# Kernel tuning notes

Measured on AMD Instinct MI355X. Metric: run time of the kernel, lower is better.

## Reference

```python
import jax, jax.numpy as jnp
import numpy as np
from jax import lax

DIM = 128; HEADS = 8; SPLIT = 4; MLP = 4
B = 8; H = 64; W = 64
EPS = 1e-5

def conv1x1(x, w, b):
    # x: (b,c,h,w), w: (o,c), b: (o,)
    return jnp.einsum('oc,bchw->bohw', w, x) + b[None, :, None, None]

def dwconv3(x, w, b):
    # depthwise 3x3, w: (C,1,3,3)
    c = x.shape[1]
    y = lax.conv_general_dilated(x, w, window_strides=(1, 1), padding=((1, 1), (1, 1)),
                                 feature_group_count=c,
                                 dimension_numbers=('NCHW', 'OIHW', 'NCHW'))
    return y + b[None, :, None, None]

def groupnorm1(x, g, bta):
    # GroupNorm with 1 group: normalize over (C,H,W) per sample
    mu = x.mean(axis=(1, 2, 3), keepdims=True)
    var = ((x - mu) ** 2).mean(axis=(1, 2, 3), keepdims=True)
    xn = (x - mu) * lax.rsqrt(var + EPS)
    return xn * g[None, :, None, None] + bta[None, :, None, None]

def eca(x, w):
    b, c, h, w_ = x.shape
    y = x.mean(axis=(2, 3))                         # (b,c)
    y = lax.conv_general_dilated(y[:, None, :], w, window_strides=(1,), padding=((2, 2),),
                                 dimension_numbers=('NCH', 'OIH', 'NCH'))  # (b,1,c)
    gate = jax.nn.sigmoid(y[:, 0])[:, :, None, None]
    return x * gate

def esa(x, alpha):
    x_se = x - x.mean(axis=(2, 3), keepdims=True)   # subtract per-channel GAP
    x_max = x_se.max(axis=1, keepdims=True)
    x_min = x_se.min(axis=1, keepdims=True)
    a = alpha[0]
    return x * jax.nn.sigmoid(x_max) * a + x * jax.nn.sigmoid(x_min) * (1.0 - a)

def eaa(q, k, v, h_sp, w_sp, cpe_w, cpe_b):
    b, c, h, w = q.shape
    hd = c // HEADS
    nh, nw = h // h_sp, w // w_sp
    L = h_sp * w_sp
    cpe = dwconv3(v, cpe_w, cpe_b)
    def win(t):
        t = t.reshape(b, c, nh, h_sp, nw, w_sp)
        t = t.transpose(0, 2, 4, 3, 5, 1).reshape(-1, L, HEADS, hd)
        return t.transpose(0, 2, 1, 3)  # (b*nh*nw, heads, L, hd)
    qw, kw, vw = win(q), win(k), win(v)
    attn = jax.nn.softmax(qw @ kw.transpose(0, 1, 3, 2), axis=-1)  # no scale, as in source
    o = attn @ vw                                    # (b*nh*nw, heads, L, hd)
    o = o.transpose(0, 2, 1, 3).reshape(b, nh, nw, h_sp, w_sp, c)
    o = o.transpose(0, 5, 1, 3, 2, 4).reshape(b, c, h, w)
    return o + cpe

def setup_inputs() -> dict:
    key = jax.random.key(0)
    ks = jax.random.split(key, 16)
    d = DIM
    z = lambda *s: jnp.zeros(s, jnp.float32)
    def n(i, shape, s=0.02):
        return jax.random.normal(ks[i], shape, dtype=jnp.float32) * s
    return dict(
        x=jax.random.normal(ks[0], (B, d, H, W), dtype=jnp.float32),
        eca_w=n(1, (1, 1, 5), 0.2),
        esa_alpha=jnp.ones((1,), jnp.float32),
        cpe1_w=n(2, (d, 1, 3, 3), 0.1), cpe1_b=z(d),
        g1=jnp.ones((d,), jnp.float32), b1=z(d),
        actp_w=n(3, (d, d)), actp_b=z(d),
        inp_w=n(4, (d, d)), inp_b=z(d),
        dwc_w=n(5, (d, 1, 3, 3), 0.1), dwc_b=z(d),
        qkv_w=n(6, (5 * d, d)), qkv_b=z(5 * d),
        eaax_w=n(7, (d, 1, 3, 3), 0.1), eaax_b=z(d),
        eaay_w=n(8, (d, 1, 3, 3), 0.1), eaay_b=z(d),
        outp_w=n(9, (d, d)), outp_b=z(d),
        cpe2_w=n(10, (d, 1, 3, 3), 0.1), cpe2_b=z(d),
        g2=jnp.ones((d,), jnp.float32), b2=z(d),
        mlp1_w=n(11, (MLP * d, d)), mlp1_b=z(MLP * d),
        mlp2_w=n(12, (d, MLP * d)), mlp2_b=z(d),
    )

def reference(x, eca_w, esa_alpha, cpe1_w, cpe1_b, g1, b1, actp_w, actp_b, inp_w, inp_b,
              dwc_w, dwc_b, qkv_w, qkv_b, eaax_w, eaax_b, eaay_w, eaay_b, outp_w, outp_b,
              cpe2_w, cpe2_b, g2, b2, mlp1_w, mlp1_b, mlp2_w, mlp2_b):
    b, c, h, w = x.shape
    x = eca(x, eca_w) + esa(x, esa_alpha)
    x = x + dwconv3(x, cpe1_w, cpe1_b)
    shortcut = x
    xn = groupnorm1(x, g1, b1)
    act_res = jax.nn.relu(conv1x1(xn, actp_w, actp_b))
    t = jax.nn.relu(dwconv3(conv1x1(xn, inp_w, inp_b), dwc_w, dwc_b))
    t = conv1x1(t, qkv_w, qkv_b)                     # (b, 5c, h, w)
    t5 = t.reshape(b, c, 5, h, w)                    # channel i::5 == t5[:,:,i]
    q0, k0, v0, q1, k1 = (t5[:, :, i] for i in range(5))
    a = eaa(q0, k0, v0, h, SPLIT, eaax_w, eaax_b) + eaa(q1, k1, v0, SPLIT, w, eaay_w, eaay_b)
    out = conv1x1(a * act_res, outp_w, outp_b) + shortcut
    out = out + dwconv3(out, cpe2_w, cpe2_b)
    mlp = conv1x1(jax.nn.relu(conv1x1(groupnorm1(out, g2, b2), mlp1_w, mlp1_b)), mlp2_w, mlp2_b)
    return mlp + out
```

## Files before the change

kernel.cpp:

```cpp
#include <hip/hip_runtime.h>

#define NPIX 4096
#define CDIM 128
#define BATCH 8
#define EPSN 1e-5f
#define LOG2E 1.44269504088896340736f

typedef __attribute__((ext_vector_type(8))) short short8;
typedef __attribute__((ext_vector_type(4))) float f32x4;
typedef __attribute__((ext_vector_type(16))) float f32x16;

__device__ __forceinline__ float sigmoidf_(float x) { return 1.f / (1.f + __expf(-x)); }

__device__ __forceinline__ unsigned short f2b(float f) {
    unsigned int u = __float_as_uint(f);
    unsigned int r = (u + 0x7FFF + ((u >> 16) & 1)) >> 16;
    return (unsigned short)r;
}
__device__ __forceinline__ float b2f(unsigned short u) {
    return __uint_as_float((unsigned int)u << 16);
}

__device__ __forceinline__ void pl32swap(unsigned int& a, unsigned int& b) {
    asm("v_permlane32_swap_b32 %0, %1" : "+v"(a), "+v"(b));
}

__device__ __forceinline__ int tok2pix(int mode, int wi, int l) {
    return (mode == 0) ? ((l >> 2) * 64 + wi * 4 + (l & 3))
                       : ((wi * 4 + (l >> 6)) * 64 + (l & 63));
}

__global__ __launch_bounds__(256) void convert_w_kernel(const float* __restrict__ qkv_w,
                                                        const float* __restrict__ mlp1_w,
                                                        const float* __restrict__ mlp2_w,
                                                        const float* __restrict__ actp_w,
                                                        const float* __restrict__ inp_w,
                                                        const float* __restrict__ outp_w,
                                                        const float* __restrict__ qkv_b,
                                                        const float* __restrict__ eaax_w,
                                                        const float* __restrict__ eaax_b,
                                                        const float* __restrict__ eaay_w,
                                                        const float* __restrict__ eaay_b,
                                                        const float* __restrict__ cpe1_w,
                                                        const float* __restrict__ dwc_w,
                                                        const float* __restrict__ cpe2_w,
                                                        const float* __restrict__ actp_b,
                                                        const float* __restrict__ inp_b,
                                                        unsigned short* __restrict__ dst,
                                                        float* __restrict__ qb_r,
                                                        float* __restrict__ wsT,
                                                        float* __restrict__ bsum,
                                                        float* __restrict__ cpe1T,
                                                        float* __restrict__ dwcT,
                                                        float* __restrict__ cpe2T,
                                                        float* __restrict__ abi,
                                                        float* __restrict__ gstats) {
    int i = blockIdx.x * 256 + threadIdx.x;
    if (i >= 267776) {
        if (i < 269824) gstats[i - 267776] = 0.f;
        return;
    }
    if (i < 262144) {
        float v;
        if (i < 81920) {
            int o = i >> 7, c = i & 127;
            int g = o >> 7;
            v = qkv_w[(size_t)(5 * (o & 127) + g) * 128 + c];
            if (g == 0 || g == 3) v *= LOG2E;
        } else if (i < 147456) v = mlp1_w[i - 81920];
        else if (i < 212992)   v = mlp2_w[i - 147456];
        else if (i < 229376)   v = actp_w[i - 212992];
        else if (i < 245760)   v = inp_w[i - 229376];
        else                   v = outp_w[i - 245760];
        dst[i] = f2b(v);
    } else {
        int j = i - 262144;
        if (j < 640) {
            int g = j >> 7;
            float v = qkv_b[5 * (j & 127) + g];
            if (g == 0 || g == 3) v *= LOG2E;
            qb_r[j] = v;
        }
        else if (j < 1792) {
            int idx = j - 640; int k = idx >> 7, c = idx & 127;
            wsT[idx] = eaax_w[c * 9 + k] + eaay_w[c * 9 + k];
        } else if (j < 1920) bsum[j - 1792] = eaax_b[j - 1792] + eaay_b[j - 1792];
        else if (j < 3072) {
            int idx = j - 1920; int k = idx >> 7, c = idx & 127;
            cpe1T[idx] = cpe1_w[c * 9 + k];
        } else if (j < 4224) {
            int idx = j - 3072; int k = idx >> 7, c = idx & 127;
            dwcT[idx] = dwc_w[c * 9 + k];
        } else if (j < 5376) {
            int idx = j - 4224; int k = idx >> 7, c = idx & 127;
            cpe2T[idx] = cpe2_w[c * 9 + k];
        } else {
            int idx = j - 5376;
            abi[idx] = (idx < 128) ? actp_b[idx] : inp_b[idx - 128];
        }
    }
}

__global__ __launch_bounds__(256) void mean_bc_kernel(const float* __restrict__ x,
                                                      float* __restrict__ mean) {
    __shared__ float sb[4];
    int bc = blockIdx.x;
    const float* p = x + (size_t)bc * NPIX;
    float s = 0.f;
    for (int i = threadIdx.x; i < NPIX; i += 256) s += p[i];
#pragma unroll
    for (int off = 32; off > 0; off >>= 1) s += __shfl_down(s, off, 64);
    if ((threadIdx.x & 63) == 0) sb[threadIdx.x >> 6] = s;
    __syncthreads();
    if (threadIdx.x == 0) mean[bc] = (sb[0] + sb[1] + sb[2] + sb[3]) * (1.f / (float)NPIX);
}

__global__ __launch_bounds__(256) void esa_tr_kernel(const float* __restrict__ x,
                                                     const float* __restrict__ mean,
                                                     const float* __restrict__ w5,
                                                     const float* __restrict__ alpha_p,
                                                     float* __restrict__ y) {
    __shared__ float tile[128][65];
    __shared__ float smx[4][64], smn[4][64], ssc[64], gat[128];
    int b = blockIdx.y, p0 = blockIdx.x * 64;
    int tx = threadIdx.x, pl = tx & 63, part = tx >> 6;
    const float* xb = x + (size_t)b * CDIM * NPIX;
    const float* mb = mean + b * CDIM;
    for (int c = part; c < CDIM; c += 4)
        tile[c][pl] = xb[(size_t)c * NPIX + p0 + pl];
    __syncthreads();
    float mx = -1e30f, mn = 1e30f;
#pragma unroll
    for (int cc = 0; cc < 32; ++cc) {
        int c = part * 32 + cc;
        float v = tile[c][pl] - mb[c];
        mx = fmaxf(mx, v); mn = fminf(mn, v);
    }
    smx[part][pl] = mx; smn[part][pl] = mn;
    __syncthreads();
    if (tx < 128) {
        float s = 0.f;
#pragma unroll
        for (int k = 0; k < 5; ++k) {
            int cc = tx + k - 2;
            if (cc >= 0 && cc < CDIM) s += w5[k] * mb[cc];
        }
        gat[tx] = sigmoidf_(s);
    }
    if (part == 0) {
        float m1 = fmaxf(fmaxf(smx[0][pl], smx[1][pl]), fmaxf(smx[2][pl], smx[3][pl]));
        float m2 = fminf(fminf(smn[0][pl], smn[1][pl]), fminf(smn[2][pl], smn[3][pl]));
        float a = alpha_p[0];
        ssc[pl] = sigmoidf_(m1) * a + sigmoidf_(m2) * (1.f - a);
    }
    __syncthreads();
    int c2 = tx & 127, pr = tx >> 7;
    float* yb = y + ((size_t)b * NPIX + p0) * CDIM;
    float gv = gat[c2];
    for (int p = pr; p < 64; p += 2)
        yb[(size_t)p * CDIM + c2] = tile[c2][p] * (gv + ssc[p]);
}

__global__ __launch_bounds__(256) void cpe_f32_kernel(const float* __restrict__ in,
                                                      const float* __restrict__ wT,
                                                      const float* __restrict__ bias,
                                                      float* __restrict__ out,
                                                      float* __restrict__ stats) {
    __shared__ float sb[8];
    int b = blockIdx.y, tx = threadIdx.x;
    int cg = tx & 15, pp = tx >> 4;
    int p = blockIdx.x * 16 + pp;
    int xx = p & 63, yy = p >> 6;
    int c0 = cg * 8;
    float acc[8], ctr[8];
#pragma unroll
    for (int j = 0; j < 8; ++j) acc[j] = bias[c0 + j];
#pragma unroll
    for (int dy = -1; dy <= 1; ++dy) {
        int y2 = yy + dy;
        if (y2 < 0 || y2 >= 64) continue;
#pragma unroll
        for (int dx = -1; dx <= 1; ++dx) {
            int x2 = xx + dx;
            if (x2 < 0 || x2 >= 64) continue;
            const float* ip = &in[((size_t)b * NPIX + y2 * 64 + x2) * 128 + c0];
            float4 v0 = *(const float4*)ip;
            float4 v1 = *(const float4*)(ip + 4);
            const float* wr = wT + ((dy + 1) * 3 + dx + 1) * 128 + c0;
            acc[0] += v0.x * wr[0]; acc[1] += v0.y * wr[1];
            acc[2] += v0.z * wr[2]; acc[3] += v0.w * wr[3];
            acc[4] += v1.x * wr[4]; acc[5] += v1.y * wr[5];
            acc[6] += v1.z * wr[6]; acc[7] += v1.w * wr[7];
            if (dy == 0 && dx == 0) {
                ctr[0] = v0.x; ctr[1] = v0.y; ctr[2] = v0.z; ctr[3] = v0.w;
                ctr[4] = v1.x; ctr[5] = v1.y; ctr[6] = v1.z; ctr[7] = v1.w;
            }
        }
    }
    float s = 0.f, s2 = 0.f;
    float r[8];
#pragma unroll
    for (int j = 0; j < 8; ++j) {
        r[j] = ctr[j] + acc[j];
        s += r[j]; s2 += r[j] * r[j];
    }
    float* op = &out[((size_t)b * NPIX + p) * 128 + c0];
    *(float4*)op = make_float4(r[0], r[1], r[2], r[3]);
    *(float4*)(op + 4) = make_float4(r[4], r[5], r[6], r[7]);
#pragma unroll
    for (int off = 32; off > 0; off >>= 1) {
        s += __shfl_down(s, off, 64);
        s2 += __shfl_down(s2, off, 64);
    }
    int wv = tx >> 6;
    if ((tx & 63) == 0) { sb[wv] = s; sb[4 + wv] = s2; }
    __syncthreads();
    if (tx == 0) {
        int slot = (b * 8 + (blockIdx.x & 7)) * 16;
        atomicAdd(&stats[slot], sb[0] + sb[1] + sb[2] + sb[3]);
        atomicAdd(&stats[slot + 1], sb[4] + sb[5] + sb[6] + sb[7]);
    }
}

__global__ __launch_bounds__(256) void dwc_bf16_kernel(const unsigned short* __restrict__ in,
                                                       const float* __restrict__ wT,
                                                       const float* __restrict__ bias,
                                                       unsigned short* __restrict__ out) {
    int b = blockIdx.y, tx = threadIdx.x;
    int cg = tx & 15, pp = tx >> 4;
    int p = blockIdx.x * 16 + pp;
    int xx = p & 63, yy = p >> 6;
    int c0 = cg * 8;
    float acc[8];
#pragma unroll
    for (int j = 0; j < 8; ++j) acc[j] = bias[c0 + j];
#pragma unroll
    for (int dy = -1; dy <= 1; ++dy) {
        int y2 = yy + dy;
        if (y2 < 0 || y2 >= 64) continue;
#pragma unroll
        for (int dx = -1; dx <= 1; ++dx) {
            int x2 = xx + dx;
            if (x2 < 0 || x2 >= 64) continue;
            unsigned short v[8];
            *(uint4*)v = *(const uint4*)&in[((size_t)b * NPIX + y2 * 64 + x2) * 128 + c0];
            const float* wr = wT + ((dy + 1) * 3 + dx + 1) * 128 + c0;
#pragma unroll
            for (int j = 0; j < 8; ++j) acc[j] += b2f(v[j]) * wr[j];
        }
    }
    unsigned short o[8];
#pragma unroll
    for (int j = 0; j < 8; ++j) o[j] = f2b(fmaxf(acc[j], 0.f));
    *(uint4*)&out[((size_t)b * NPIX + p) * 128 + c0] = *(uint4*)o;
}

__global__ __launch_bounds__(256) void conv_mfma_kernel(const unsigned short* __restrict__ in_t,
                                                        const float* __restrict__ in_f32,
                                                        const float* __restrict__ gst,
                                                        const float* __restrict__ gg,
                                                        const float* __restrict__ gbta,
                                                        const unsigned short* __restrict__ w,
                                                        const float* __restrict__ bias,
                                                        const float* __restrict__ res,
                                                        float* __restrict__ out,
                                                        unsigned short* __restrict__ out_t,
                                                        unsigned short* __restrict__ out_t2,
                                                        int Cin, int Cout, int relu, int nchw) {
    __shared__ __align__(16) unsigned short A_s[128][136];
    __shared__ __align__(16) unsigned short B_s[64][136];
    int b = blockIdx.z, p0 = blockIdx.x * 64, o0 = blockIdx.y * 128;
    int tx = threadIdx.x;
    int wave = tx >> 6, lane = tx & 63;
    int wm = wave & 1, wn = wave >> 1;
    int quad = lane >> 4, l16 = lane & 15;

    float mu = 0.f, rr = 1.f;
    if (in_f32) {
        float su = 0.f, sq = 0.f;
#pragma unroll
        for (int sl = 0; sl < 8; ++sl) {
            su += gst[(b * 8 + sl) * 16];
            sq += gst[(b * 8 + sl) * 16 + 1];
        }
        const float n = 1.f / (float)(CDIM * NPIX);
        mu = su * n;
        float var = sq * n - mu * mu;
        rr = rsqrtf(var + EPSN);
    }

    f32x4 acc[4][2];
#pragma unroll
    for (int mt = 0; mt < 4; ++mt) {
#pragma unroll
        for (int r = 0; r < 4; ++r) {
            float bv = bias[o0 + wm * 64 + mt * 16 + quad * 4 + r];
#pragma unroll
            for (int nt = 0; nt < 2; ++nt) acc[mt][nt][r] = bv;
        }
    }

    for (int k0 = 0; k0 < Cin; k0 += 128) {
#pragma unroll
        for (int j = 0; j < 8; ++j) {
            int idx = tx + 256 * j;
            int row = idx >> 4, c16 = idx & 15;
            *(uint4*)&A_s[row][c16 * 8] =
                *(const uint4*)&w[(size_t)(o0 + row) * Cin + k0 + c16 * 8];
        }
        if (in_f32) {
#pragma unroll
            for (int j = 0; j < 4; ++j) {
                int idx = tx + 256 * j;
                int row = idx >> 4, c16 = idx & 15;
                int ch = c16 * 8;
                const float* ip = &in_f32[((size_t)b * NPIX + p0 + row) * 128 + ch];
                float4 v0 = *(const float4*)ip;
                float4 v1 = *(const float4*)(ip + 4);
                unsigned short o[8];
                o[0] = f2b((v0.x - mu) * rr * gg[ch + 0] + gbta[ch + 0]);
                o[1] = f2b((v0.y - mu) * rr * gg[ch + 1] + gbta[ch + 1]);
                o[2] = f2b((v0.z - mu) * rr * gg[ch + 2] + gbta[ch + 2]);
                o[3] = f2b((v0.w - mu) * rr * gg[ch + 3] + gbta[ch + 3]);
                o[4] = f2b((v1.x - mu) * rr * gg[ch + 4] + gbta[ch + 4]);
                o[5] = f2b((v1.y - mu) * rr * gg[ch + 5] + gbta[ch + 5]);
                o[6] = f2b((v1.z - mu) * rr * gg[ch + 6] + gbta[ch + 6]);
                o[7] = f2b((v1.w - mu) * rr * gg[ch + 7] + gbta[ch + 7]);
                *(uint4*)&B_s[row][c16 * 8] = *(uint4*)o;
            }
        } else {
#pragma unroll
            for (int j = 0; j < 4; ++j) {
                int idx = tx + 256 * j;
                int row = idx >> 4, c16 = idx & 15;
                *(uint4*)&B_s[row][c16 * 8] =
                    *(const uint4*)&in_t[((size_t)b * NPIX + p0 + row) * Cin + k0 + c16 * 8];
            }
        }
        __syncthreads();
#pragma unroll
        for (int ks = 0; ks < 128; ks += 32) {
            short8 af[4], bf[2];
#pragma unroll
            for (int mt = 0; mt < 4; ++mt)
                af[mt] = *(const short8*)&A_s[wm * 64 + mt * 16 + l16][ks + quad * 8];
#pragma unroll
            for (int nt = 0; nt < 2; ++nt)
                bf[nt] = *(const short8*)&B_s[wn * 32 + nt * 16 + l16][ks + quad * 8];
#pragma unroll
            for (int mt = 0; mt < 4; ++mt)
#pragma unroll
                for (int nt = 0; nt < 2; ++nt)
                    acc[mt][nt] = __builtin_amdgcn_mfma_f32_16x16x32_bf16(
                        af[mt], bf[nt], acc[mt][nt], 0, 0, 0);
        }
        __syncthreads();
    }

    int dorelu = (relu == 1) || (relu == 2 && blockIdx.y == 0);
    if (out_t) {
#pragma unroll
        for (int mt = 0; mt < 4; ++mt) {
#pragma unroll
            for (int nt = 0; nt < 2; ++nt) {
                int p = p0 + wn * 32 + nt * 16 + l16;
                int ob = o0 + wm * 64 + mt * 16 + quad * 4;
                unsigned short* dbuf = out_t;
                int oc = ob;
                if (out_t2 && o0 >= 128) { dbuf = out_t2; oc = ob - 128; }
                ushort4 u;
                float v0 = acc[mt][nt][0], v1 = acc[mt][nt][1];
                float v2 = acc[mt][nt][2], v3 = acc[mt][nt][3];
                if (dorelu) { v0 = fmaxf(v0, 0.f); v1 = fmaxf(v1, 0.f);
                              v2 = fmaxf(v2, 0.f); v3 = fmaxf(v3, 0.f); }
                u.x = f2b(v0); u.y = f2b(v1); u.z = f2b(v2); u.w = f2b(v3);
                *(ushort4*)&dbuf[((size_t)b * NPIX + p) * Cout + oc] = u;
            }
        }
    } else if (!nchw) {
#pragma unroll
        for (int mt = 0; mt < 4; ++mt) {
#pragma unroll
            for (int nt = 0; nt < 2; ++nt) {
                int p = p0 + wn * 32 + nt * 16 + l16;
                int ob = o0 + wm * 64 + mt * 16 + quad * 4;
                size_t ix = ((size_t)b * NPIX + p) * Cout + ob;
                float4 v = make_float4(acc[mt][nt][0], acc[mt][nt][1],
                                       acc[mt][nt][2], acc[mt][nt][3]);
                if (dorelu) { v.x = fmaxf(v.x, 0.f); v.y = fmaxf(v.y, 0.f);
                              v.z = fmaxf(v.z, 0.f); v.w = fmaxf(v.w, 0.f); }
                if (res) {
                    float4 rv = *(const float4*)&res[ix];
                    v.x += rv.x; v.y += rv.y; v.z += rv.z; v.w += rv.w;
                }
                *(float4*)&out[ix] = v;
            }
        }
    } else {
        float* outb = out + (size_t)b * Cout * NPIX;
#pragma unroll
        for (int mt = 0; mt < 4; ++mt) {
#pragma unroll
            for (int nt = 0; nt < 2; ++nt) {
                int p = p0 + wn * 32 + nt * 16 + l16;
                int ob = o0 + wm * 64 + mt * 16 + quad * 4;
                float4 rv = make_float4(0.f, 0.f, 0.f, 0.f);
                if (res) rv = *(const float4*)&res[((size_t)b * NPIX + p) * 128 + ob];
#pragma unroll
                for (int r = 0; r < 4; ++r) {
                    float v = acc[mt][nt][r];
                    if (dorelu) v = fmaxf(v, 0.f);
                    v += (r == 0 ? rv.x : r == 1 ? rv.y : r == 2 ? rv.z : rv.w);
                    outb[(size_t)(ob + r) * NPIX + p] = v;
                }
            }
        }
    }
}

__global__ __launch_bounds__(256) void attn_dual_kernel(const unsigned short* __restrict__ t_t,
                                                        float* __restrict__ a0,
                                                        float* __restrict__ a1) {
    __shared__ __align__(16) unsigned short Vt[32][264];
    int wi = blockIdx.x, head = blockIdx.y;
    int z = blockIdx.z;
    int b = z >> 1, which = z & 1;
    int qoff = which ? 384 : 0;
    int koff = which ? 512 : 128;
    int mode = which;
    float* a_out = which ? a1 : a0;
    int tx = threadIdx.x;
    int wave = tx >> 6, l = tx & 63;
    int l32 = l & 31, half = l >> 5;
    const size_t base = (size_t)b * NPIX;
    const int hc = head * 16;

    {
        int p = tok2pix(mode, wi, tx);
        const unsigned short* vp = &t_t[(base + p) * 640 + 256 + hc];
        unsigned short tmp[16];
        *(uint4*)&tmp[0] = *(const uint4*)vp;
        *(uint4*)&tmp[8] = *(const uint4*)(vp + 8);
#pragma unroll
        for (int d = 0; d < 16; ++d) Vt[d][tx] = tmp[d];
        Vt[16][tx] = (unsigned short)0x3F80;
#pragma unroll
        for (int d = 17; d < 32; ++d) Vt[d][tx] = 0;
    }
    __syncthreads();

    f32x16 zzero;
#pragma unroll
    for (int r = 0; r < 16; ++r) zzero[r] = 0.f;

    int pofs[8];
#pragma unroll
    for (int nt = 0; nt < 8; ++nt)
        pofs[nt] = tok2pix(mode, wi, nt * 32 + l32) * 640;

    const unsigned short* tb = t_t + base * 640 + hc + half * 8;
    const unsigned short* kb = tb + koff;
    const unsigned short* qb = tb + qoff;

#pragma unroll
    for (int qi = 0; qi < 2; ++qi) {
        int qs = qi * 4 + wave;
        int qp = tok2pix(mode, wi, qs * 32 + l32);
        short8 qf = *(const short8*)&qb[(size_t)qp * 640];
        f32x16 o_acc = zzero;
#pragma unroll
        for (int nt = 0; nt < 8; ++nt) {
            short8 kf = *(const short8*)&kb[pofs[nt]];
            f32x16 s = __builtin_amdgcn_mfma_f32_32x32x16_bf16(kf, qf, zzero, 0, 0, 0);
            unsigned int pk[8];
#pragma unroll
            for (int i = 0; i < 8; ++i) {
                float e0 = __builtin_amdgcn_exp2f(s[2 * i]);
                float e1 = __builtin_amdgcn_exp2f(s[2 * i + 1]);
                pk[i] = __builtin_amdgcn_perm(__float_as_uint(e1), __float_as_uint(e0),
                                              0x07060302u);
            }
            pl32swap(pk[0], pk[2]);
            pl32swap(pk[1], pk[3]);
            pl32swap(pk[4], pk[6]);
            pl32swap(pk[5], pk[7]);
            short8 vf0 = *(const short8*)&Vt[l32][nt * 32 + half * 8];
            short8 vf1 = *(const short8*)&Vt[l32][nt * 32 + 16 + half * 8];
            unsigned int u0[4] = {pk[0], pk[1], pk[2], pk[3]};
            unsigned int u1[4] = {pk[4], pk[5], pk[6], pk[7]};
            o_acc = __builtin_amdgcn_mfma_f32_32x32x16_bf16(vf0, *(short8*)u0, o_acc, 0, 0, 0);
            o_acc = __builtin_amdgcn_mfma_f32_32x32x16_bf16(vf1, *(short8*)u1, o_acc, 0, 0, 0);
        }
        float rs = o_acc[8];
        rs += __shfl_xor(rs, 32, 64);
        float rinv = 1.f / rs;
        float* dst = a_out + (base + qp) * 128 + hc + 4 * half;
        float4 s0 = make_float4(o_acc[0] * rinv, o_acc[1] * rinv,
                                o_acc[2] * rinv, o_acc[3] * rinv);
        float4 s1 = make_float4(o_acc[4] * rinv, o_acc[5] * rinv,
                                o_acc[6] * rinv, o_acc[7] * rinv);
        *(float4*)dst = s0;
        *(float4*)(dst + 8) = s1;
    }
}

__global__ __launch_bounds__(256) void mul3_cpe_kernel(const float* __restrict__ a0,
                                                       const float* __restrict__ a1,
                                                       const unsigned short* __restrict__ act,
                                                       const unsigned short* __restrict__ t_t,
                                                       const float* __restrict__ wT,
                                                       const float* __restrict__ bsum,
                                                       unsigned short* __restrict__ dst) {
    int b = blockIdx.y;
    int tx = threadIdx.x;
    int cg = tx & 15, pp = tx >> 4;
    int p = blockIdx.x * 16 + pp;
    int xx = p & 63, yy = p >> 6;
    int c0 = cg * 8;
    float acc[8];
#pragma unroll
    for (int j = 0; j < 8; ++j) acc[j] = bsum[c0 + j];
#pragma unroll
    for (int dy = -1; dy <= 1; ++dy) {
        int y2 = yy + dy;
        if (y2 < 0 || y2 >= 64) continue;
#pragma unroll
        for (int dx = -1; dx <= 1; ++dx) {
            int x2 = xx + dx;
            if (x2 < 0 || x2 >= 64) continue;
            int pn = y2 * 64 + x2;
            unsigned short v[8];
            *(uint4*)v = *(const uint4*)&t_t[((size_t)b * NPIX + pn) * 640 + 256 + c0];
            const float* wr = wT + ((dy + 1) * 3 + dx + 1) * 128 + c0;
#pragma unroll
            for (int j = 0; j < 8; ++j) acc[j] += b2f(v[j]) * wr[j];
        }
    }
    size_t base = ((size_t)b * NPIX + p) * 128 + c0;
    float4 x0 = *(const float4*)&a0[base];
    float4 x1 = *(const float4*)&a0[base + 4];
    float4 y0 = *(const float4*)&a1[base];
    float4 y1 = *(const float4*)&a1[base + 4];
    unsigned short t[8];
    *(uint4*)t = *(const uint4*)&act[base];
    unsigned short r[8];
    r[0] = f2b((x0.x + y0.x + acc[0]) * b2f(t[0]));
    r[1] = f2b((x0.y + y0.y + acc[1]) * b2f(t[1]));
    r[2] = f2b((x0.z + y0.z + acc[2]) * b2f(t[2]));
    r[3] = f2b((x0.w + y0.w + acc[3]) * b2f(t[3]));
    r[4] = f2b((x1.x + y1.x + acc[4]) * b2f(t[4]));
    r[5] = f2b((x1.y + y1.y + acc[5]) * b2f(t[5]));
    r[6] = f2b((x1.z + y1.z + acc[6]) * b2f(t[6]));
    r[7] = f2b((x1.w + y1.w + acc[7]) * b2f(t[7]));
    *(uint4*)&dst[base] = *(uint4*)r;
}

extern "C" void kernel_launch(void* const* d_in, const int* in_sizes, int n_in,
                              void* d_out, int out_size, void* d_ws, size_t ws_size,
                              hipStream_t stream) {
    const float* x       = (const float*)d_in[0];
    const float* eca_w   = (const float*)d_in[1];
    const float* esa_al  = (const float*)d_in[2];
    const float* cpe1_w  = (const float*)d_in[3];  const float* cpe1_b = (const float*)d_in[4];
    const float* g1      = (const float*)d_in[5];  const float* b1     = (const float*)d_in[6];
    const float* actp_w  = (const float*)d_in[7];  const float* actp_b = (const float*)d_in[8];
    const float* inp_w   = (const float*)d_in[9];  const float* inp_b  = (const float*)d_in[10];
    const float* dwc_w   = (const float*)d_in[11]; const float* dwc_b  = (const float*)d_in[12];
    const float* qkv_w   = (const float*)d_in[13]; const float* qkv_b  = (const float*)d_in[14];
    const float* eaax_w  = (const float*)d_in[15]; const float* eaax_b = (const float*)d_in[16];
    const float* eaay_w  = (const float*)d_in[17]; const float* eaay_b = (const float*)d_in[18];
    const float* outp_w  = (const float*)d_in[19]; const float* outp_b = (const float*)d_in[20];
    const float* cpe2_w  = (const float*)d_in[21]; const float* cpe2_b = (const float*)d_in[22];
    const float* g2      = (const float*)d_in[23]; const float* b2     = (const float*)d_in[24];
    const float* mlp1_w  = (const float*)d_in[25]; const float* mlp1_b = (const float*)d_in[26];
    const float* mlp2_w  = (const float*)d_in[27]; const float* mlp2_b = (const float*)d_in[28];

    float* ws = (float*)d_ws;
    unsigned short* U = (unsigned short*)d_ws;
    const size_t E = (size_t)BATCH * CDIM * NPIX;

    float* y_nhwc  = ws;
    float* a0      = ws;
    float* sc_nhwc = ws + E;
    unsigned short* act_t = U + 5 * E;
    unsigned short* it_t  = U + 6 * E;
    unsigned short* tin_t = U + 7 * E;
    float* a1      = ws + 4 * E;
    unsigned short* t_t   = U + 10 * E;
    unsigned short* m_t   = U + 15 * E;
    float* out_nhwc = ws + 8 * E;
    float* out2    = ws + 2 * E;
    unsigned short* hid_t = U + 10 * E;
    unsigned short* wpool = U + 20 * E;
    unsigned short* wq  = wpool;
    unsigned short* wm1 = wpool + 81920;
    unsigned short* wm2 = wpool + 147456;
    unsigned short* wai = wpool + 212992;
    unsigned short* wo  = wpool + 245760;
    float* fb     = ws + 10 * E + 131072;
    float* meanb  = fb;
    float* gstats = fb + 2048;
    float* qb_r   = fb + 4096;
    float* wsT    = fb + 4736;
    float* bsum   = fb + 5888;
    float* cpe1T  = fb + 6016;
    float* dwcT   = fb + 7168;
    float* cpe2T  = fb + 8320;
    float* abi    = fb + 9472;

    convert_w_kernel<<<1054, 256, 0, stream>>>(qkv_w, mlp1_w, mlp2_w, actp_w, inp_w, outp_w,
                                               qkv_b, eaax_w, eaax_b, eaay_w, eaay_b,
                                               cpe1_w, dwc_w, cpe2_w, actp_b, inp_b,
                                               wpool, qb_r, wsT, bsum, cpe1T, dwcT, cpe2T, abi,
                                               gstats);

    mean_bc_kernel<<<BATCH * CDIM, 256, 0, stream>>>(x, meanb);
    esa_tr_kernel<<<dim3(64, BATCH), 256, 0, stream>>>(x, meanb, eca_w, esa_al, y_nhwc);
    cpe_f32_kernel<<<dim3(256, BATCH), 256, 0, stream>>>(y_nhwc, cpe1T, cpe1_b, sc_nhwc, gstats);
    conv_mfma_kernel<<<dim3(64, 2, BATCH), 256, 0, stream>>>(nullptr, sc_nhwc, gstats, g1, b1,
                                                             wai, abi, nullptr, nullptr,
                                                             act_t, it_t, 128, 128, 2, 0);
    dwc_bf16_kernel<<<dim3(256, BATCH), 256, 0, stream>>>(it_t, dwcT, dwc_b, tin_t);
    conv_mfma_kernel<<<dim3(64, 5, BATCH), 256, 0, stream>>>(tin_t, nullptr, nullptr, nullptr,
                                                             nullptr, wq, qb_r, nullptr, nullptr,
                                                             t_t, nullptr, 128, 640, 0, 0);
    attn_dual_kernel<<<dim3(16, 8, 2 * BATCH), 256, 0, stream>>>(t_t, a0, a1);
    mul3_cpe_kernel<<<dim3(256, BATCH), 256, 0, stream>>>(a0, a1, act_t, t_t, wsT, bsum, m_t);
    conv_mfma_kernel<<<dim3(64, 1, BATCH), 256, 0, stream>>>(m_t, nullptr, nullptr, nullptr,
                                                             nullptr, wo, outp_b, sc_nhwc,
                                                             out_nhwc, nullptr, nullptr,
                                                             128, 128, 0, 0);
    cpe_f32_kernel<<<dim3(256, BATCH), 256, 0, stream>>>(out_nhwc, cpe2T, cpe2_b, out2,
                                                         gstats + 1024);
    conv_mfma_kernel<<<dim3(64, 4, BATCH), 256, 0, stream>>>(nullptr, out2, gstats + 1024, g2, b2,
                                                             wm1, mlp1_b, nullptr, nullptr,
                                                             hid_t, nullptr, 128, 512, 1, 0);
    conv_mfma_kernel<<<dim3(64, 1, BATCH), 256, 0, stream>>>(hid_t, nullptr, nullptr, nullptr,
                                                             nullptr, wm2, mlp2_b, out2,
                                                             (float*)d_out, nullptr, nullptr,
                                                             512, 128, 0, 1);
}
```

Before: 300.0 us.

## Loop over output-channel tiles inside conv blocks to reuse the staged input tile

The 1x1 MFMA conv kernel now iterates over all 128-wide output-channel tiles inside one block instead of spreading them across blockIdx.y. For Cin==128 the input tile, including the fused GroupNorm normalization and bf16 conversion, is loaded into LDS once and reused for every output tile. This removes redundant input reads and repeated normalization work. In exchange the grid shrinks to 512 blocks, which cuts parallelism and latency hiding on a GPU with many CUs.

```diff
diff --git a/kernel.cpp b/kernel.cpp
--- a/kernel.cpp
+++ b/kernel.cpp
@@ -266,10 +266,11 @@
                                                         float* __restrict__ out,
                                                         unsigned short* __restrict__ out_t,
                                                         unsigned short* __restrict__ out_t2,
-                                                        int Cin, int Cout, int relu, int nchw) {
+                                                        int Cin, int Cout, int relu, int nchw,
+                                                        int ntile) {
     __shared__ __align__(16) unsigned short A_s[128][136];
     __shared__ __align__(16) unsigned short B_s[64][136];
-    int b = blockIdx.z, p0 = blockIdx.x * 64, o0 = blockIdx.y * 128;
+    int b = blockIdx.z, p0 = blockIdx.x * 64;
     int tx = threadIdx.x;
     int wave = tx >> 6, lane = tx & 63;
     int wm = wave & 1, wn = wave >> 1;
@@ -289,25 +290,7 @@
         rr = rsqrtf(var + EPSN);
     }
 
-    f32x4 acc[4][2];
-#pragma unroll
-    for (int mt = 0; mt < 4; ++mt) {
-#pragma unroll
-        for (int r = 0; r < 4; ++r) {
-            float bv = bias[o0 + wm * 64 + mt * 16 + quad * 4 + r];
-#pragma unroll
-            for (int nt = 0; nt < 2; ++nt) acc[mt][nt][r] = bv;
-        }
-    }
-
-    for (int k0 = 0; k0 < Cin; k0 += 128) {
-#pragma unroll
-        for (int j = 0; j < 8; ++j) {
-            int idx = tx + 256 * j;
-            int row = idx >> 4, c16 = idx & 15;
-            *(uint4*)&A_s[row][c16 * 8] =
-                *(const uint4*)&w[(size_t)(o0 + row) * Cin + k0 + c16 * 8];
-        }
+    if (Cin == 128) {
         if (in_f32) {
 #pragma unroll
             for (int j = 0; j < 4; ++j) {
@@ -334,84 +317,118 @@
                 int idx = tx + 256 * j;
                 int row = idx >> 4, c16 = idx & 15;
                 *(uint4*)&B_s[row][c16 * 8] =
-                    *(const uint4*)&in_t[((size_t)b * NPIX + p0 + row) * Cin + k0 + c16 * 8];
-            }
-        }
-        __syncthreads();
-#pragma unroll
-        for (int ks = 0; ks < 128; ks += 32) {
-            short8 af[4], bf[2];
-#pragma unroll
-            for (int mt = 0; mt < 4; ++mt)
-                af[mt] = *(const short8*)&A_s[wm * 64 + mt * 16 + l16][ks + quad * 8];
-#pragma unroll
-            for (int nt = 0; nt < 2; ++nt)
-                bf[nt] = *(const short8*)&B_s[wn * 32 + nt * 16 + l16][ks + quad * 8];
-#pragma unroll
-            for (int mt = 0; mt < 4; ++mt)
+                    *(const uint4*)&in_t[((size_t)b * NPIX + p0 + row) * Cin + c16 * 8];
+            }
+        }
+    }
+
+    for (int t = 0; t < ntile; ++t) {
+        int o0 = t * 128;
+
+        f32x4 acc[4][2];
+#pragma unroll
+        for (int mt = 0; mt < 4; ++mt) {
+#pragma unroll
+            for (int r = 0; r < 4; ++r) {
+                float bv = bias[o0 + wm * 64 + mt * 16 + quad * 4 + r];
+#pragma unroll
+                for (int nt = 0; nt < 2; ++nt) acc[mt][nt][r] = bv;
+            }
+        }
+
+        for (int k0 = 0; k0 < Cin; k0 += 128) {
+#pragma unroll
+            for (int j = 0; j < 8; ++j) {
+                int idx = tx + 256 * j;
+                int row = idx >> 4, c16 = idx & 15;
+                *(uint4*)&A_s[row][c16 * 8] =
+                    *(const uint4*)&w[(size_t)(o0 + row) * Cin + k0 + c16 * 8];
+            }
+            if (Cin != 128) {
+#pragma unroll
+                for (int j = 0; j < 4; ++j) {
+                    int idx = tx + 256 * j;
+                    int row = idx >> 4, c16 = idx & 15;
+                    *(uint4*)&B_s[row][c16 * 8] =
+                        *(const uint4*)&in_t[((size_t)b * NPIX + p0 + row) * Cin + k0 + c16 * 8];
+                }
+            }
+            __syncthreads();
+#pragma unroll
+            for (int ks = 0; ks < 128; ks += 32) {
+                short8 af[4], bf[2];
+#pragma unroll
+                for (int mt = 0; mt < 4; ++mt)
+                    af[mt] = *(const short8*)&A_s[wm * 64 + mt * 16 + l16][ks + quad * 8];
 #pragma unroll
                 for (int nt = 0; nt < 2; ++nt)
-                    acc[mt][nt] = __builtin_amdgcn_mfma_f32_16x16x32_bf16(
-                        af[mt], bf[nt], acc[mt][nt], 0, 0, 0);
-        }
-        __syncthreads();
-    }
-
-    int dorelu = (relu == 1) || (relu == 2 && blockIdx.y == 0);
-    if (out_t) {
-#pragma unroll
-        for (int mt = 0; mt < 4; ++mt) {
-#pragma unroll
-            for (int nt = 0; nt < 2; ++nt) {
-                int p = p0 + wn * 32 + nt * 16 + l16;
-                int ob = o0 + wm * 64 + mt * 16 + quad * 4;
-                unsigned short* dbuf = out_t;
-                int oc = ob;
-                if (out_t2 && o0 >= 128) { dbuf = out_t2; oc = ob - 128; }
-                ushort4 u;
-                float v0 = acc[mt][nt][0], v1 = acc[mt][nt][1];
-                float v2 = acc[mt][nt][2], v3 = acc[mt][nt][3];
-                if (dorelu) { v0 = fmaxf(v0, 0.f); v1 = fmaxf(v1, 0.f);
-                              v2 = fmaxf(v2, 0.f); v3 = fmaxf(v3, 0.f); }
-                u.x = f2b(v0); u.y = f2b(v1); u.z = f2b(v2); u.w = f2b(v3);
-                *(ushort4*)&dbuf[((size_t)b * NPIX + p) * Cout + oc] = u;
-            }
-        }
-    } else if (!nchw) {
-#pragma unroll
-        for (int mt = 0; mt < 4; ++mt) {
-#pragma unroll
-            for (int nt = 0; nt < 2; ++nt) {
-                int p = p0 + wn * 32 + nt * 16 + l16;
-                int ob = o0 + wm * 64 + mt * 16 + quad * 4;
-                size_t ix = ((size_t)b * NPIX + p) * Cout + ob;
-                float4 v = make_float4(acc[mt][nt][0], acc[mt][nt][1],
-                                       acc[mt][nt][2], acc[mt][nt][3]);
-                if (dorelu) { v.x = fmaxf(v.x, 0.f); v.y = fmaxf(v.y, 0.f);
-                              v.z = fmaxf(v.z, 0.f); v.w = fmaxf(v.w, 0.f); }
-                if (res) {
-                    float4 rv = *(const float4*)&res[ix];
-                    v.x += rv.x; v.y += rv.y; v.z += rv.z; v.w += rv.w;
+                    bf[nt] = *(const short8*)&B_s[wn * 32 + nt * 16 + l16][ks + quad * 8];
+#pragma unroll
+                for (int mt = 0; mt < 4; ++mt)
+#pragma unroll
+                    for (int nt = 0; nt < 2; ++nt)
+                        acc[mt][nt] = __builtin_amdgcn_mfma_f32_16x16x32_bf16(
+                            af[mt], bf[nt], acc[mt][nt], 0, 0, 0);
+            }
+            __syncthreads();
+        }
+
+        int dorelu = (relu == 1) || (relu == 2 && t == 0);
+        if (out_t) {
+#pragma unroll
+            for (int mt = 0; mt < 4; ++mt) {
+#pragma unroll
+                for (int nt = 0; nt < 2; ++nt) {
+                    int p = p0 + wn * 32 + nt * 16 + l16;
+                    int ob = o0 + wm * 64 + mt * 16 + quad * 4;
+                    unsigned short* dbuf = out_t;
+                    int oc = ob;
+                    if (out_t2 && o0 >= 128) { dbuf = out_t2; oc = ob - 128; }
+                    ushort4 u;
+                    float v0 = acc[mt][nt][0], v1 = acc[mt][nt][1];
+                    float v2 = acc[mt][nt][2], v3 = acc[mt][nt][3];
+                    if (dorelu) { v0 = fmaxf(v0, 0.f); v1 = fmaxf(v1, 0.f);
+                                  v2 = fmaxf(v2, 0.f); v3 = fmaxf(v3, 0.f); }
+                    u.x = f2b(v0); u.y = f2b(v1); u.z = f2b(v2); u.w = f2b(v3);
+                    *(ushort4*)&dbuf[((size_t)b * NPIX + p) * Cout + oc] = u;
                 }
-                *(float4*)&out[ix] = v;
-            }
-        }
-    } else {
-        float* outb = out + (size_t)b * Cout * NPIX;
-#pragma unroll
-        for (int mt = 0; mt < 4; ++mt) {
-#pragma unroll
-            for (int nt = 0; nt < 2; ++nt) {
-                int p = p0 + wn * 32 + nt * 16 + l16;
-                int ob = o0 + wm * 64 + mt * 16 + quad * 4;
-                float4 rv = make_float4(0.f, 0.f, 0.f, 0.f);
-                if (res) rv = *(const float4*)&res[((size_t)b * NPIX + p) * 128 + ob];
-#pragma unroll
-                for (int r = 0; r < 4; ++r) {
-                    float v = acc[mt][nt][r];
-                    if (dorelu) v = fmaxf(v, 0.f);
-                    v += (r == 0 ? rv.x : r == 1 ? rv.y : r == 2 ? rv.z : rv.w);
-                    outb[(size_t)(ob + r) * NPIX + p] = v;
+            }
+        } else if (!nchw) {
+#pragma unroll
+            for (int mt = 0; mt < 4; ++mt) {
+#pragma unroll
+                for (int nt = 0; nt < 2; ++nt) {
+                    int p = p0 + wn * 32 + nt * 16 + l16;
+                    int ob = o0 + wm * 64 + mt * 16 + quad * 4;
+                    size_t ix = ((size_t)b * NPIX + p) * Cout + ob;
+                    float4 v = make_float4(acc[mt][nt][0], acc[mt][nt][1],
+                                           acc[mt][nt][2], acc[mt][nt][3]);
+                    if (dorelu) { v.x = fmaxf(v.x, 0.f); v.y = fmaxf(v.y, 0.f);
+                                  v.z = fmaxf(v.z, 0.f); v.w = fmaxf(v.w, 0.f); }
+                    if (res) {
+                        float4 rv = *(const float4*)&res[ix];
+                        v.x += rv.x; v.y += rv.y; v.z += rv.z; v.w += rv.w;
+                    }
+                    *(float4*)&out[ix] = v;
+                }
+            }
+        } else {
+            float* outb = out + (size_t)b * Cout * NPIX;
+#pragma unroll
+            for (int mt = 0; mt < 4; ++mt) {
+#pragma unroll
+                for (int nt = 0; nt < 2; ++nt) {
+                    int p = p0 + wn * 32 + nt * 16 + l16;
+                    int ob = o0 + wm * 64 + mt * 16 + quad * 4;
+                    float4 rv = make_float4(0.f, 0.f, 0.f, 0.f);
+                    if (res) rv = *(const float4*)&res[((size_t)b * NPIX + p) * 128 + ob];
+#pragma unroll
+                    for (int r = 0; r < 4; ++r) {
+                        float v = acc[mt][nt][r];
+                        if (dorelu) v = fmaxf(v, 0.f);
+                        v += (r == 0 ? rv.x : r == 1 ? rv.y : r == 2 ? rv.z : rv.w);
+                        outb[(size_t)(ob + r) * NPIX + p] = v;
+                    }
                 }
             }
         }
@@ -617,26 +634,26 @@
     mean_bc_kernel<<<BATCH * CDIM, 256, 0, stream>>>(x, meanb);
     esa_tr_kernel<<<dim3(64, BATCH), 256, 0, stream>>>(x, meanb, eca_w, esa_al, y_nhwc);
     cpe_f32_kernel<<<dim3(256, BATCH), 256, 0, stream>>>(y_nhwc, cpe1T, cpe1_b, sc_nhwc, gstats);
-    conv_mfma_kernel<<<dim3(64, 2, BATCH), 256, 0, stream>>>(nullptr, sc_nhwc, gstats, g1, b1,
+    conv_mfma_kernel<<<dim3(64, 1, BATCH), 256, 0, stream>>>(nullptr, sc_nhwc, gstats, g1, b1,
                                                              wai, abi, nullptr, nullptr,
-                                                             act_t, it_t, 128, 128, 2, 0);
+                                                             act_t, it_t, 128, 128, 2, 0, 2);
     dwc_bf16_kernel<<<dim3(256, BATCH), 256, 0, stream>>>(it_t, dwcT, dwc_b, tin_t);
-    conv_mfma_kernel<<<dim3(64, 5, BATCH), 256, 0, stream>>>(tin_t, nullptr, nullptr, nullptr,
+    conv_mfma_kernel<<<dim3(64, 1, BATCH), 256, 0, stream>>>(tin_t, nullptr, nullptr, nullptr,
                                                              nullptr, wq, qb_r, nullptr, nullptr,
-                                                             t_t, nullptr, 128, 640, 0, 0);
+                                                             t_t, nullptr, 128, 640, 0, 0, 5);
     attn_dual_kernel<<<dim3(16, 8, 2 * BATCH), 256, 0, stream>>>(t_t, a0, a1);
     mul3_cpe_kernel<<<dim3(256, BATCH), 256, 0, stream>>>(a0, a1, act_t, t_t, wsT, bsum, m_t);
     conv_mfma_kernel<<<dim3(64, 1, BATCH), 256, 0, stream>>>(m_t, nullptr, nullptr, nullptr,
                                                              nullptr, wo, outp_b, sc_nhwc,
                                                              out_nhwc, nullptr, nullptr,
-                                                             128, 128, 0, 0);
+                                                             128, 128, 0, 0, 1);
     cpe_f32_kernel<<<dim3(256, BATCH), 256, 0, stream>>>(out_nhwc, cpe2T, cpe2_b, out2,
                                                          gstats + 1024);
-    conv_mfma_kernel<<<dim3(64, 4, BATCH), 256, 0, stream>>>(nullptr, out2, gstats + 1024, g2, b2,
+    conv_mfma_kernel<<<dim3(64, 1, BATCH), 256, 0, stream>>>(nullptr, out2, gstats + 1024, g2, b2,
                                                              wm1, mlp1_b, nullptr, nullptr,
-                                                             hid_t, nullptr, 128, 512, 1, 0);
+                                                             hid_t, nullptr, 128, 512, 1, 0, 4);
     conv_mfma_kernel<<<dim3(64, 1, BATCH), 256, 0, stream>>>(hid_t, nullptr, nullptr, nullptr,
                                                              nullptr, wm2, mlp2_b, out2,
                                                              (float*)d_out, nullptr, nullptr,
-                                                             512, 128, 0, 1);
-}
+                                                             512, 128, 0, 1, 1);
+}
```

After: 322.7 us. 7.6% more time.
